# Kernel optimization log

Hardware: AMD Instinct MI355X
Metric: run time of the kernel (lower is better)

Reference implementation:

```python
import jax, jax.numpy as jnp
import numpy as np


def setup_inputs() -> dict:
    key = jax.random.key(0)
    ks = jax.random.split(key, 13)
    HID = 256
    N = 2 * HID                      # hidden_dim * 2
    B_DOC, S, T_K = 32, 40, 64      # docs, sentences/doc, max words/sentence
    B_SENT = B_DOC * S               # total sentences = sum(sent_lens)
    MAX_DOC_LEN = S * T_K
    f = jnp.float32
    sc = jnp.float32(0.05)
    sent_lens = jnp.full((B_DOC,), S, dtype=jnp.int32)
    inp = {
        "s_t_hat": jax.random.normal(ks[0], (B_DOC, N), f),
        "encoder_outputs": jax.random.normal(ks[1], (B_SENT, T_K, N), f),
        "encoder_feature": jax.random.normal(ks[2], (B_SENT * T_K, N), f) * jnp.float32(0.5),
        "seq_lens2": jax.random.randint(ks[3], (B_SENT,), T_K // 2, T_K + 1, dtype=jnp.int32),
        "sent_s_t_hat": jax.random.normal(ks[4], (B_DOC, N), f),
        "sent_enc_outputs": jax.random.normal(ks[5], (B_DOC, S, N), f),
        "sent_enc_feature": jax.random.normal(ks[6], (B_DOC * S, N), f) * jnp.float32(0.5),
        "sent_enc_padding_mask": (jnp.arange(S)[None, :] < sent_lens[:, None]).astype(f),
        "sent_lens": sent_lens,
        "max_doc_len": MAX_DOC_LEN,
        "coverage": jnp.zeros((B_SENT, T_K), f),
        "Wd": jax.random.normal(ks[7], (N, N), f) * sc,
        "bd": jax.random.normal(ks[8], (N,), f) * sc,
        "v_w": jax.random.normal(ks[9], (N,), f) * sc,
        "Wsd": jax.random.normal(ks[10], (N, N), f) * sc,
        "bsd": jax.random.normal(ks[11], (N,), f) * sc,
        "sv_w": jax.random.normal(ks[12], (N,), f) * sc,
    }
    return inp


def _excl_cumsum(x):
    return jnp.cumsum(x) - x


def reference(s_t_hat, encoder_outputs, encoder_feature, seq_lens2, sent_s_t_hat,
              sent_enc_outputs, sent_enc_feature, sent_enc_padding_mask, sent_lens,
              max_doc_len, coverage, Wd, bd, v_w, Wsd, bsd, sv_w):
    B_SENT, T_K, N = encoder_outputs.shape
    B_DOC, S, _ = sent_enc_outputs.shape
    dtype = encoder_outputs.dtype

    # sentence s -> owning doc (replaces first Python loop: broadcast dec_fea per doc)
    doc_ids = jnp.repeat(jnp.arange(B_DOC), sent_lens, total_repeat_length=B_SENT)

    # ---- word-level additive attention over each sentence ----
    dec_fea = s_t_hat @ Wd + bd                              # [B_DOC, N]
    att = jnp.tanh(encoder_feature.reshape(B_SENT, T_K, N) + dec_fea[doc_ids][:, None, :])
    scores = att @ v_w                                        # [B_SENT, T_K]
    w_mask = (jnp.arange(T_K)[None, :] < seq_lens2[:, None]).astype(dtype)
    w_attn_ = jax.nn.softmax(scores, axis=1) * w_mask
    w_attn = w_attn_ / w_attn_.sum(1, keepdims=True)          # [B_SENT, T_K]

    # ---- sentence-level additive attention over each doc ----
    sent_dec_fea = sent_s_t_hat @ Wsd + bsd                   # [B_DOC, N]
    sent_att = jnp.tanh(sent_enc_feature.reshape(B_DOC, S, N) + sent_dec_fea[:, None, :])
    sent_scores = sent_att @ sv_w                             # [B_DOC, S]
    sent_attn_ = jax.nn.softmax(sent_scores, axis=1) * sent_enc_padding_mask
    sent_attn_dist = sent_attn_ / sent_attn_.sum(1, keepdims=True)

    # ---- ragged flatten: scatter valid words of each sentence into its doc stream ----
    sent_start = _excl_cumsum(sent_lens)                      # first sentence idx per doc
    sent_local = jnp.arange(B_SENT) - sent_start[doc_ids]     # sentence pos within doc
    mult_attn = sent_attn_dist[doc_ids, sent_local][:, None] * w_attn  # [B_SENT, T_K]

    word_cum = _excl_cumsum(seq_lens2)                        # global word offsets
    doc_word_off = word_cum - word_cum[sent_start[doc_ids]]   # offset within doc
    pos = doc_word_off[:, None] + jnp.arange(T_K)[None, :]    # [B_SENT, T_K]
    valid = jnp.arange(T_K)[None, :] < seq_lens2[:, None]
    flat = jnp.where(valid, doc_ids[:, None] * max_doc_len + pos, B_DOC * max_doc_len)
    flat = flat.reshape(-1)

    enc_output2 = (jnp.zeros((B_DOC * max_doc_len, N), dtype)
                   .at[flat].set(encoder_outputs.reshape(-1, N), mode="drop")
                   .reshape(B_DOC, max_doc_len, N))
    attn_dist_sw = (jnp.zeros((B_DOC * max_doc_len,), dtype)
                    .at[flat].set(mult_attn.reshape(-1), mode="drop")
                    .reshape(B_DOC, max_doc_len))

    c_t = jnp.einsum("bl,bln->bn", attn_dist_sw, enc_output2)  # [B_DOC, N]
    return (c_t, attn_dist_sw, coverage, sent_attn_dist)
```

## Files before the change

### kernel.cpp

```cpp
#include <hip/hip_runtime.h>
#include <hip/hip_bf16.h>
#include <math.h>

#define B_DOC 32
#define S_MAX 40
#define T_K 64
#define N_DIM 512
#define B_SENT (B_DOC * S_MAX)
#define MAXDOC (S_MAX * T_K)
#define KCHUNK 4

__device__ __forceinline__ float fast_tanh(float x) {
    float e = __expf(2.0f * x);
    return 1.0f - 2.0f * __builtin_amdgcn_rcpf(e + 1.0f);
}

__global__ __launch_bounds__(256) void prep_fea_kernel(
        const int* __restrict__ seq_lens2, const int* __restrict__ sent_lens,
        const float* __restrict__ s_t_hat, const float* __restrict__ sent_s_t_hat,
        const float* __restrict__ Wd, const float* __restrict__ bd,
        const float* __restrict__ Wsd, const float* __restrict__ bsd,
        float* __restrict__ fea_part,
        int* __restrict__ doc_ids, int* __restrict__ sent_local,
        int* __restrict__ doc_word_off, int* __restrict__ sent_start_g,
        int* __restrict__ doc_words_total) {
    int tid = threadIdx.x;
    if (blockIdx.x == 0) {
        __shared__ int ss[B_DOC + 1];
        __shared__ int wc[B_SENT + 1];
        __shared__ int wsum[4];
        int lane = tid & 63, w = tid >> 6;

        int ls[5];
        #pragma unroll
        for (int k = 0; k < 5; ++k) ls[k] = seq_lens2[tid * 5 + k];
        int sum = ls[0] + ls[1] + ls[2] + ls[3] + ls[4];

        int scan = sum;
        #pragma unroll
        for (int off = 1; off < 64; off <<= 1) {
            int v = __shfl_up(scan, off, 64);
            if (lane >= off) scan += v;
        }
        if (lane == 63) wsum[w] = scan;

        if (w == 0) {
            int sl = (lane < B_DOC) ? sent_lens[lane] : 0;
            int sc2 = sl;
            #pragma unroll
            for (int off = 1; off < 64; off <<= 1) {
                int v = __shfl_up(sc2, off, 64);
                if (lane >= off) sc2 += v;
            }
            if (lane < B_DOC) ss[lane + 1] = sc2;
            if (lane == 0) ss[0] = 0;
        }
        __syncthreads();

        int wbase = 0;
        for (int i = 0; i < w; ++i) wbase += wsum[i];
        int excl = wbase + scan - sum;
        #pragma unroll
        for (int k = 0; k < 5; ++k) { wc[tid * 5 + k] = excl; excl += ls[k]; }
        if (tid == 255) wc[B_SENT] = excl;
        __syncthreads();

        if (tid <= B_DOC) sent_start_g[tid] = ss[tid];
        if (tid < B_DOC) doc_words_total[tid] = wc[ss[tid + 1]] - wc[ss[tid]];

        for (int i = tid; i < B_SENT; i += 256) {
            int lo = 0, hi = B_DOC - 1;
            while (lo < hi) { int mid = (lo + hi + 1) >> 1; if (ss[mid] <= i) lo = mid; else hi = mid - 1; }
            doc_ids[i] = lo;
            sent_local[i] = i - ss[lo];
            doc_word_off[i] = wc[i] - wc[ss[lo]];
        }
    } else {
        int blk = blockIdx.x - 1;
        int c = blk & (KCHUNK - 1);
        int b = (blk >> 2) & 31;
        int m = blk >> 7;
        const int KC = N_DIM / KCHUNK;
        const float* x = (m ? sent_s_t_hat : s_t_hat) + b * N_DIM + c * KC;
        const float* W = (m ? Wsd : Wd) + (size_t)c * KC * N_DIM;
        const float* bias = (m ? bsd : bd);
        float* out = fea_part + ((size_t)(m * 32 + b) * KCHUNK + c) * N_DIM;
        __shared__ float xs[128];
        if (tid < KC) xs[tid] = x[tid];
        __syncthreads();
        float a0 = 0.f, a1 = 0.f;
        if (c == 0) { a0 = bias[tid]; a1 = bias[tid + 256]; }
        #pragma unroll 8
        for (int k = 0; k < KC; ++k) {
            float xv = xs[k];
            a0 = fmaf(xv, W[k * N_DIM + tid], a0);
            a1 = fmaf(xv, W[k * N_DIM + tid + 256], a1);
        }
        out[tid] = a0;
        out[tid + 256] = a1;
    }
}

__global__ __launch_bounds__(256, 4) void fused_kernel(
        const float* __restrict__ ef, const float* __restrict__ eo,
        const float* __restrict__ sef, const float* __restrict__ fea_part,
        const float* __restrict__ v_w, const float* __restrict__ sv_w,
        const float* __restrict__ mask, const int* __restrict__ seq_lens2,
        const int* __restrict__ doc_ids,
        float* __restrict__ part, float* __restrict__ wn,
        float* __restrict__ o_sent) {
    int tid = threadIdx.x;
    int w = tid >> 6, lane = tid & 63;

    if (blockIdx.x < B_DOC) {
        int doc = blockIdx.x;
        __shared__ __align__(16) float df[N_DIM];
        __shared__ __align__(16) float vw[N_DIM];
        __shared__ float sc2[S_MAX];
        const float* fp = fea_part + (size_t)(32 + doc) * KCHUNK * N_DIM;
        for (int i = tid; i < N_DIM; i += 256) {
            df[i] = fp[i] + fp[N_DIM + i] + fp[2 * N_DIM + i] + fp[3 * N_DIM + i];
            vw[i] = sv_w[i];
        }
        __syncthreads();
        const float4* sef4 = (const float4*)(sef + (size_t)doc * S_MAX * N_DIM);
        const float4* df4 = (const float4*)df;
        const float4* vw4 = (const float4*)vw;
        for (int t = w; t < S_MAX; t += 4) {
            float acc = 0.0f;
            #pragma unroll
            for (int j = 0; j < 2; ++j) {
                int n4 = lane + 64 * j;
                float4 e = sef4[t * 128 + n4];
                float4 d = df4[n4];
                float4 v = vw4[n4];
                acc = fmaf(v.x, fast_tanh(e.x + d.x), acc);
                acc = fmaf(v.y, fast_tanh(e.y + d.y), acc);
                acc = fmaf(v.z, fast_tanh(e.z + d.z), acc);
                acc = fmaf(v.w, fast_tanh(e.w + d.w), acc);
            }
            #pragma unroll
            for (int off = 32; off >= 1; off >>= 1) acc += __shfl_xor(acc, off, 64);
            if (lane == 0) sc2[t] = acc;
        }
        __syncthreads();
        if (tid < 64) {
            bool valid = tid < S_MAX;
            float x = valid ? sc2[tid] : -INFINITY;
            float m = x;
            #pragma unroll
            for (int off = 32; off >= 1; off >>= 1) m = fmaxf(m, __shfl_xor(m, off, 64));
            float mk = valid ? mask[doc * S_MAX + tid] : 0.0f;
            float e = valid ? __expf(x - m) * mk : 0.0f;
            float ssum = e;
            #pragma unroll
            for (int off = 32; off >= 1; off >>= 1) ssum += __shfl_xor(ssum, off, 64);
            if (valid) o_sent[doc * S_MAX + tid] = e / ssum;
        }
        return;
    }

    int s = blockIdx.x - B_DOC;
    int h = lane >> 5, sub = lane & 31;
    __shared__ float sc[T_K];
    __shared__ float wl[4];
    __shared__ __align__(16) float4 red[4][128];

    int doc = doc_ids[s];
    int len = seq_lens2[s];

    const float4* fp4 = (const float4*)(fea_part + (size_t)doc * KCHUNK * N_DIM);
    const float4* vw4 = (const float4*)v_w;
    float4 d[4], v[4];
    #pragma unroll
    for (int k = 0; k < 4; ++k) {
        int j = sub + 32 * k;
        float4 a = fp4[j], b = fp4[128 + j], c = fp4[256 + j], e = fp4[384 + j];
        d[k].x = a.x + b.x + c.x + e.x;
        d[k].y = a.y + b.y + c.y + e.y;
        d[k].z = a.z + b.z + c.z + e.z;
        d[k].w = a.w + b.w + c.w + e.w;
        v[k] = vw4[j];
    }

    const float4* ef4 = (const float4*)ef + (size_t)s * T_K * 128;
    const float4* eo4 = (const float4*)eo + (size_t)s * T_K * 128;

    float l_w = 0.0f;
    float4 O[4];
    #pragma unroll
    for (int k = 0; k < 4; ++k) O[k] = (float4){0.f, 0.f, 0.f, 0.f};

    int t = 2 * w;
    float4 ea[4];
    {
        int row = t + h;
        #pragma unroll
        for (int k = 0; k < 4; ++k) ea[k] = ef4[row * 128 + sub + 32 * k];
    }
    for (; t < len; t += 8) {
        int row = t + h;
        float4 p4[4];
        #pragma unroll
        for (int k = 0; k < 4; ++k) p4[k] = eo4[row * 128 + sub + 32 * k];
        float4 eb[4];
        int tn = t + 8;
        if (tn < len) {
            int rown = tn + h;
            #pragma unroll
            for (int k = 0; k < 4; ++k) eb[k] = ef4[rown * 128 + sub + 32 * k];
        }
        float a0, a1, a2, a3;
        a0  = v[0].x * fast_tanh(ea[0].x + d[0].x);
        a1  = v[1].x * fast_tanh(ea[1].x + d[1].x);
        a2  = v[2].x * fast_tanh(ea[2].x + d[2].x);
        a3  = v[3].x * fast_tanh(ea[3].x + d[3].x);
        a0 = fmaf(v[0].y, fast_tanh(ea[0].y + d[0].y), a0);
        a1 = fmaf(v[1].y, fast_tanh(ea[1].y + d[1].y), a1);
        a2 = fmaf(v[2].y, fast_tanh(ea[2].y + d[2].y), a2);
        a3 = fmaf(v[3].y, fast_tanh(ea[3].y + d[3].y), a3);
        a0 = fmaf(v[0].z, fast_tanh(ea[0].z + d[0].z), a0);
        a1 = fmaf(v[1].z, fast_tanh(ea[1].z + d[1].z), a1);
        a2 = fmaf(v[2].z, fast_tanh(ea[2].z + d[2].z), a2);
        a3 = fmaf(v[3].z, fast_tanh(ea[3].z + d[3].z), a3);
        a0 = fmaf(v[0].w, fast_tanh(ea[0].w + d[0].w), a0);
        a1 = fmaf(v[1].w, fast_tanh(ea[1].w + d[1].w), a1);
        a2 = fmaf(v[2].w, fast_tanh(ea[2].w + d[2].w), a2);
        a3 = fmaf(v[3].w, fast_tanh(ea[3].w + d[3].w), a3);
        float acc = (a0 + a1) + (a2 + a3);
        #pragma unroll
        for (int off = 16; off >= 1; off >>= 1) acc += __shfl_xor(acc, off, 64);
        bool valid = (t + h) < len;
        if (sub == 0 && valid) sc[t + h] = acc;
        float p = valid ? __expf(acc) : 0.0f;
        l_w += p;
        #pragma unroll
        for (int k = 0; k < 4; ++k) {
            O[k].x = fmaf(p, p4[k].x, O[k].x);
            O[k].y = fmaf(p, p4[k].y, O[k].y);
            O[k].z = fmaf(p, p4[k].z, O[k].z);
            O[k].w = fmaf(p, p4[k].w, O[k].w);
        }
        #pragma unroll
        for (int k = 0; k < 4; ++k) ea[k] = eb[k];
    }

    l_w += __shfl_xor(l_w, 32, 64);
    #pragma unroll
    for (int k = 0; k < 4; ++k) {
        O[k].x += __shfl_xor(O[k].x, 32, 64);
        O[k].y += __shfl_xor(O[k].y, 32, 64);
        O[k].z += __shfl_xor(O[k].z, 32, 64);
        O[k].w += __shfl_xor(O[k].w, 32, 64);
    }
    if (lane == 0) wl[w] = l_w;
    if (h == 0) {
        #pragma unroll
        for (int k = 0; k < 4; ++k) red[w][sub + 32 * k] = O[k];
    }
    __syncthreads();

    float l = (wl[0] + wl[1]) + (wl[2] + wl[3]);
    float inv = 1.0f / l;
    if (tid < 128) {
        float4 a = red[0][tid], b = red[1][tid], c = red[2][tid], e = red[3][tid];
        float4 r = {(a.x + b.x + c.x + e.x) * inv, (a.y + b.y + c.y + e.y) * inv,
                    (a.z + b.z + c.z + e.z) * inv, (a.w + b.w + c.w + e.w) * inv};
        ((float4*)(part + (size_t)s * N_DIM))[tid] = r;
    }
    if (tid < T_K && tid < len) wn[s * T_K + tid] = __expf(sc[tid]) * inv;
}

__global__ __launch_bounds__(256) void finalize_kernel(
        const float* __restrict__ part, const float* __restrict__ wn,
        const float* __restrict__ o_sent, const int* __restrict__ seq_lens2,
        const int* __restrict__ sent_start, const int* __restrict__ doc_word_off,
        const int* __restrict__ doc_words_total, const int* __restrict__ mdl,
        const float* __restrict__ cov_in,
        float* __restrict__ c_t, float* __restrict__ out_attn,
        float* __restrict__ out_cov) {
    int doc = blockIdx.x;
    int tid = threadIdx.x;
    int maxdoc = mdl[0];
    __shared__ float sa_sh[S_MAX];
    int st = sent_start[doc], en = sent_start[doc + 1];
    int ns = en - st;
    if (tid < S_MAX) sa_sh[tid] = o_sent[doc * S_MAX + tid];

    {
        const float4* ci = (const float4*)cov_in;
        float4* co = (float4*)out_cov;
        int n4 = (B_SENT * T_K) / 4;
        for (int i = doc * 256 + tid; i < n4; i += 32 * 256)
            co[i] = ci[i];
    }
    __syncthreads();

    if (tid < 128) {
        float4 acc = {0.f, 0.f, 0.f, 0.f};
        for (int i = 0; i < ns; ++i) {
            float sa = sa_sh[i];
            float4 p = ((const float4*)(part + (size_t)(st + i) * N_DIM))[tid];
            acc.x = fmaf(sa, p.x, acc.x);
            acc.y = fmaf(sa, p.y, acc.y);
            acc.z = fmaf(sa, p.z, acc.z);
            acc.w = fmaf(sa, p.w, acc.w);
        }
        ((float4*)(c_t + (size_t)doc * N_DIM))[tid] = acc;
    }

    int w = tid >> 6, lane = tid & 63;
    for (int i = w; i < ns; i += 4) {
        int s = st + i;
        int len = seq_lens2[s];
        float sa = sa_sh[i];
        if (lane < len)
            out_attn[(size_t)doc * maxdoc + doc_word_off[s] + lane] =
                sa * wn[s * T_K + lane];
    }
    int dwt = doc_words_total[doc];
    for (int i = dwt + tid; i < maxdoc; i += 256)
        out_attn[(size_t)doc * maxdoc + i] = 0.0f;
}

extern "C" void kernel_launch(void* const* d_in, const int* in_sizes, int n_in,
                              void* d_out, int out_size, void* d_ws, size_t ws_size,
                              hipStream_t stream) {
    const float* s_t_hat        = (const float*)d_in[0];
    const float* encoder_out    = (const float*)d_in[1];
    const float* encoder_feat   = (const float*)d_in[2];
    const int*   seq_lens2      = (const int*)d_in[3];
    const float* sent_s_t_hat   = (const float*)d_in[4];
    const float* sent_enc_feat  = (const float*)d_in[6];
    const float* sent_pad_mask  = (const float*)d_in[7];
    const int*   sent_lens      = (const int*)d_in[8];
    const int*   max_doc_len    = (const int*)d_in[9];
    const float* coverage       = (const float*)d_in[10];
    const float* Wd             = (const float*)d_in[11];
    const float* bd             = (const float*)d_in[12];
    const float* v_w            = (const float*)d_in[13];
    const float* Wsd            = (const float*)d_in[14];
    const float* bsd            = (const float*)d_in[15];
    const float* sv_w           = (const float*)d_in[16];

    float* out      = (float*)d_out;
    float* o_ct     = out;
    float* o_attn   = out + B_DOC * N_DIM;
    float* o_cov    = o_attn + B_DOC * MAXDOC;
    float* o_sent   = o_cov + B_SENT * T_K;

    float* ws          = (float*)d_ws;
    float* fea_part    = ws;
    float* part        = ws + 131072;
    float* wn          = ws + 131072 + 655360;
    int*   ints        = (int*)(ws + 131072 + 655360 + 81920);
    int*   doc_ids     = ints;
    int*   sent_local  = ints + B_SENT;
    int*   doc_w_off   = ints + 2 * B_SENT;
    int*   sent_start  = ints + 3 * B_SENT;
    int*   doc_wtot    = ints + 3 * B_SENT + 33;

    prep_fea_kernel<<<257, 256, 0, stream>>>(seq_lens2, sent_lens, s_t_hat,
                                             sent_s_t_hat, Wd, bd, Wsd, bsd,
                                             fea_part, doc_ids, sent_local,
                                             doc_w_off, sent_start, doc_wtot);
    fused_kernel<<<B_SENT + B_DOC, 256, 0, stream>>>(encoder_feat, encoder_out,
                                                     sent_enc_feat, fea_part,
                                                     v_w, sv_w, sent_pad_mask,
                                                     seq_lens2, doc_ids,
                                                     part, wn, o_sent);
    finalize_kernel<<<B_DOC, 256, 0, stream>>>(part, wn, o_sent, seq_lens2,
                                               sent_start, doc_w_off, doc_wtot,
                                               max_doc_len, coverage,
                                               o_ct, o_attn, o_cov);
}
```

Before: 67.97 us.

## Split each sentence's word attention across two blocks with deferred normalization

The word-attention part of the fused kernel now launches two blocks per sentence, each covering 32 of the 64 word positions. Each block writes its unnormalized context vector and exp-sum to the workspace, and the finalize kernel combines the two halves and applies normalization. The aim is more parallelism and shorter per-block serial loops, since the stream over encoder features and outputs runs on twice as many blocks. The cost is twice the partial-context traffic and per-block setup, plus more work in the single-block-per-doc finalize kernel. Softmax uses exp without max subtraction, unchanged from before.

```diff
diff --git a/kernel.cpp b/kernel.cpp
--- a/kernel.cpp
+++ b/kernel.cpp
@@ -107,8 +107,8 @@
         const float* __restrict__ v_w, const float* __restrict__ sv_w,
         const float* __restrict__ mask, const int* __restrict__ seq_lens2,
         const int* __restrict__ doc_ids,
-        float* __restrict__ part, float* __restrict__ wn,
-        float* __restrict__ o_sent) {
+        float* __restrict__ part, float* __restrict__ lsum,
+        float* __restrict__ wn, float* __restrict__ o_sent) {
     int tid = threadIdx.x;
     int w = tid >> 6, lane = tid & 63;
 
@@ -160,14 +160,17 @@
         return;
     }
 
-    int s = blockIdx.x - B_DOC;
-    int h = lane >> 5, sub = lane & 31;
-    __shared__ float sc[T_K];
+    int idx = blockIdx.x - B_DOC;
+    int s = idx >> 1;
+    int half = idx & 1;
+    int B0 = half * 32;
+    int hh = lane >> 5, sub = lane & 31;
     __shared__ float wl[4];
     __shared__ __align__(16) float4 red[4][128];
 
     int doc = doc_ids[s];
     int len = seq_lens2[s];
+    int te = min(len, B0 + 32);
 
     const float4* fp4 = (const float4*)(fea_part + (size_t)doc * KCHUNK * N_DIM);
     const float4* vw4 = (const float4*)v_w;
@@ -191,22 +194,22 @@
     #pragma unroll
     for (int k = 0; k < 4; ++k) O[k] = (float4){0.f, 0.f, 0.f, 0.f};
 
-    int t = 2 * w;
+    int t = B0 + 2 * w;
     float4 ea[4];
     {
-        int row = t + h;
+        int row = t + hh;
         #pragma unroll
         for (int k = 0; k < 4; ++k) ea[k] = ef4[row * 128 + sub + 32 * k];
     }
-    for (; t < len; t += 8) {
-        int row = t + h;
+    for (; t < te; t += 8) {
+        int row = t + hh;
         float4 p4[4];
         #pragma unroll
         for (int k = 0; k < 4; ++k) p4[k] = eo4[row * 128 + sub + 32 * k];
         float4 eb[4];
         int tn = t + 8;
-        if (tn < len) {
-            int rown = tn + h;
+        if (tn < te) {
+            int rown = tn + hh;
             #pragma unroll
             for (int k = 0; k < 4; ++k) eb[k] = ef4[rown * 128 + sub + 32 * k];
         }
@@ -230,9 +233,9 @@
         float acc = (a0 + a1) + (a2 + a3);
         #pragma unroll
         for (int off = 16; off >= 1; off >>= 1) acc += __shfl_xor(acc, off, 64);
-        bool valid = (t + h) < len;
-        if (sub == 0 && valid) sc[t + h] = acc;
+        bool valid = (t + hh) < te;
         float p = valid ? __expf(acc) : 0.0f;
+        if (sub == 0 && valid) wn[s * T_K + t + hh] = p;
         l_w += p;
         #pragma unroll
         for (int k = 0; k < 4; ++k) {
@@ -254,38 +257,43 @@
         O[k].w += __shfl_xor(O[k].w, 32, 64);
     }
     if (lane == 0) wl[w] = l_w;
-    if (h == 0) {
+    if (hh == 0) {
         #pragma unroll
         for (int k = 0; k < 4; ++k) red[w][sub + 32 * k] = O[k];
     }
     __syncthreads();
 
-    float l = (wl[0] + wl[1]) + (wl[2] + wl[3]);
-    float inv = 1.0f / l;
+    if (tid == 0) lsum[idx] = (wl[0] + wl[1]) + (wl[2] + wl[3]);
     if (tid < 128) {
         float4 a = red[0][tid], b = red[1][tid], c = red[2][tid], e = red[3][tid];
-        float4 r = {(a.x + b.x + c.x + e.x) * inv, (a.y + b.y + c.y + e.y) * inv,
-                    (a.z + b.z + c.z + e.z) * inv, (a.w + b.w + c.w + e.w) * inv};
-        ((float4*)(part + (size_t)s * N_DIM))[tid] = r;
-    }
-    if (tid < T_K && tid < len) wn[s * T_K + tid] = __expf(sc[tid]) * inv;
+        float4 r = {a.x + b.x + c.x + e.x, a.y + b.y + c.y + e.y,
+                    a.z + b.z + c.z + e.z, a.w + b.w + c.w + e.w};
+        ((float4*)(part + (size_t)idx * N_DIM))[tid] = r;
+    }
 }
 
 __global__ __launch_bounds__(256) void finalize_kernel(
-        const float* __restrict__ part, const float* __restrict__ wn,
-        const float* __restrict__ o_sent, const int* __restrict__ seq_lens2,
-        const int* __restrict__ sent_start, const int* __restrict__ doc_word_off,
-        const int* __restrict__ doc_words_total, const int* __restrict__ mdl,
-        const float* __restrict__ cov_in,
+        const float* __restrict__ part, const float* __restrict__ lsum,
+        const float* __restrict__ wn, const float* __restrict__ o_sent,
+        const int* __restrict__ seq_lens2, const int* __restrict__ sent_start,
+        const int* __restrict__ doc_word_off, const int* __restrict__ doc_words_total,
+        const int* __restrict__ mdl, const float* __restrict__ cov_in,
         float* __restrict__ c_t, float* __restrict__ out_attn,
         float* __restrict__ out_cov) {
     int doc = blockIdx.x;
     int tid = threadIdx.x;
     int maxdoc = mdl[0];
     __shared__ float sa_sh[S_MAX];
+    __shared__ float linv_sh[S_MAX];
     int st = sent_start[doc], en = sent_start[doc + 1];
     int ns = en - st;
-    if (tid < S_MAX) sa_sh[tid] = o_sent[doc * S_MAX + tid];
+    if (tid < S_MAX) {
+        sa_sh[tid] = o_sent[doc * S_MAX + tid];
+        if (tid < ns) {
+            float l = lsum[2 * (st + tid)] + lsum[2 * (st + tid) + 1];
+            linv_sh[tid] = 1.0f / l;
+        }
+    }
 
     {
         const float4* ci = (const float4*)cov_in;
@@ -299,12 +307,13 @@
     if (tid < 128) {
         float4 acc = {0.f, 0.f, 0.f, 0.f};
         for (int i = 0; i < ns; ++i) {
-            float sa = sa_sh[i];
-            float4 p = ((const float4*)(part + (size_t)(st + i) * N_DIM))[tid];
-            acc.x = fmaf(sa, p.x, acc.x);
-            acc.y = fmaf(sa, p.y, acc.y);
-            acc.z = fmaf(sa, p.z, acc.z);
-            acc.w = fmaf(sa, p.w, acc.w);
+            float w0 = sa_sh[i] * linv_sh[i];
+            float4 pa = ((const float4*)(part + (size_t)(2 * (st + i)) * N_DIM))[tid];
+            float4 pb = ((const float4*)(part + (size_t)(2 * (st + i) + 1) * N_DIM))[tid];
+            acc.x = fmaf(w0, pa.x + pb.x, acc.x);
+            acc.y = fmaf(w0, pa.y + pb.y, acc.y);
+            acc.z = fmaf(w0, pa.z + pb.z, acc.z);
+            acc.w = fmaf(w0, pa.w + pb.w, acc.w);
         }
         ((float4*)(c_t + (size_t)doc * N_DIM))[tid] = acc;
     }
@@ -313,10 +322,10 @@
     for (int i = w; i < ns; i += 4) {
         int s = st + i;
         int len = seq_lens2[s];
-        float sa = sa_sh[i];
+        float w0 = sa_sh[i] * linv_sh[i];
         if (lane < len)
             out_attn[(size_t)doc * maxdoc + doc_word_off[s] + lane] =
-                sa * wn[s * T_K + lane];
+                w0 * wn[s * T_K + lane];
     }
     int dwt = doc_words_total[doc];
     for (int i = dwt + tid; i < maxdoc; i += 256)
@@ -352,8 +361,9 @@
     float* ws          = (float*)d_ws;
     float* fea_part    = ws;
     float* part        = ws + 131072;
-    float* wn          = ws + 131072 + 655360;
-    int*   ints        = (int*)(ws + 131072 + 655360 + 81920);
+    float* wn          = ws + 131072 + 1310720;
+    float* lsum        = wn + 81920;
+    int*   ints        = (int*)(lsum + 2560);
     int*   doc_ids     = ints;
     int*   sent_local  = ints + B_SENT;
     int*   doc_w_off   = ints + 2 * B_SENT;
@@ -364,12 +374,12 @@
                                              sent_s_t_hat, Wd, bd, Wsd, bsd,
                                              fea_part, doc_ids, sent_local,
                                              doc_w_off, sent_start, doc_wtot);
-    fused_kernel<<<B_SENT + B_DOC, 256, 0, stream>>>(encoder_feat, encoder_out,
-                                                     sent_enc_feat, fea_part,
-                                                     v_w, sv_w, sent_pad_mask,
-                                                     seq_lens2, doc_ids,
-                                                     part, wn, o_sent);
-    finalize_kernel<<<B_DOC, 256, 0, stream>>>(part, wn, o_sent, seq_lens2,
+    fused_kernel<<<B_DOC + 2 * B_SENT, 256, 0, stream>>>(encoder_feat, encoder_out,
+                                                         sent_enc_feat, fea_part,
+                                                         v_w, sv_w, sent_pad_mask,
+                                                         seq_lens2, doc_ids,
+                                                         part, lsum, wn, o_sent);
+    finalize_kernel<<<B_DOC, 256, 0, stream>>>(part, lsum, wn, o_sent, seq_lens2,
                                                sent_start, doc_w_off, doc_wtot,
                                                max_doc_len, coverage,
                                                o_ct, o_attn, o_cov);
```

New measurement: 72.64 us. 1.07x slower.
